# Optimization experiments

Measured on AMD Instinct MI355X. Metric: run time of the kernel, lower is better.

The kernel has to match this reference:

```python
import jax, jax.numpy as jnp
import numpy as np

D_MODEL = 1024
N_HEADS = 16
D_K = 64
BATCH = 2
SEQ = 2048
LN_EPS = 1e-5


def setup_inputs() -> dict:
    key = jax.random.key(0)
    ks = jax.random.split(key, 6)
    s = 1.0 / np.sqrt(D_MODEL)
    return {
        "h": jax.random.normal(ks[0], (BATCH, SEQ, D_MODEL), dtype=jnp.float32),
        "Wq": jax.random.normal(ks[1], (D_MODEL, D_MODEL), dtype=jnp.float32) * s,
        "bq": jnp.zeros((D_MODEL,), jnp.float32),
        "Wk": jax.random.normal(ks[2], (D_MODEL, D_MODEL), dtype=jnp.float32) * s,
        "bk": jnp.zeros((D_MODEL,), jnp.float32),
        "Wv": jax.random.normal(ks[3], (D_MODEL, D_MODEL), dtype=jnp.float32) * s,
        "bv": jnp.zeros((D_MODEL,), jnp.float32),
        "Wo": jax.random.normal(ks[4], (D_MODEL, D_MODEL), dtype=jnp.float32) * s,
        "bo": jnp.zeros((D_MODEL,), jnp.float32),
        "ln_w": jnp.ones((D_MODEL,), jnp.float32),
        "ln_b": jnp.zeros((D_MODEL,), jnp.float32),
    }


def _layernorm(x, w, b):
    mu = jnp.mean(x, axis=-1, keepdims=True)
    var = jnp.var(x, axis=-1, keepdims=True)
    return (x - mu) * jax.lax.rsqrt(var + LN_EPS) * w + b


def reference(h, Wq, bq, Wk, bk, Wv, bv, Wo, bo, ln_w, ln_b):
    b, s, _ = h.shape
    scale = 1.0 / np.sqrt(D_K)
    h_res = h
    hn = _layernorm(h, ln_w, ln_b)
    # Linear layers (torch convention: y = x @ W.T + b), split into heads
    q = (hn @ Wq.T + bq).reshape(b, s, N_HEADS, D_K)
    k = (hn @ Wk.T + bk).reshape(b, s, N_HEADS, D_K)
    v = (hn @ Wv.T + bv).reshape(b, s, N_HEADS, D_K)
    attn = jnp.einsum('bihd,bjhd->bhij', q, k) * scale  # [b, h, i, j]
    attn = jax.nn.softmax(attn, axis=-1)
    o = jnp.einsum('bhij,bjhd->bihd', attn, v).reshape(b, s, N_HEADS * D_K)
    out = o @ Wo.T + bo
    return out + h_res
```

## Files before the change

kernel.cpp:

```cpp
#include <hip/hip_runtime.h>
#include <cstdint>

#define D_MODEL 1024
#define N_HEADS 16
#define D_K     64
#define BATCH   2
#define SEQ     2048
#define TOKENS  (BATCH * SEQ)
#define LN_EPS  1e-5f
#define QSCALE  0.18033688011112042f

typedef __bf16 bf16x8 __attribute__((ext_vector_type(8)));
typedef float  floatx4  __attribute__((ext_vector_type(4)));
typedef float  floatx16 __attribute__((ext_vector_type(16)));

__device__ __forceinline__ unsigned short f2bf(float f) {
  union { float f; unsigned u; } v; v.f = f;
  unsigned r = v.u + 0x7fffu + ((v.u >> 16) & 1u);
  return (unsigned short)(r >> 16);
}
__device__ __forceinline__ unsigned pk2bf(float hi, float lo) {
  union { float f; unsigned u; } a, b;
  a.f = hi; b.f = lo;
  return __builtin_amdgcn_perm(a.u, b.u, 0x07060302u);
}

__device__ __forceinline__ void cp16(void* lds, const void* g) {
  __builtin_amdgcn_global_load_lds(
      (__attribute__((address_space(1))) void*)g,
      (__attribute__((address_space(3))) void*)lds, 16, 0, 0);
}

__global__ __launch_bounds__(256) void prep_kernel(
    const float* __restrict__ h, const float* __restrict__ w0,
    const float* __restrict__ w1, const float* __restrict__ w2,
    const float* __restrict__ w3, const float* __restrict__ lw,
    const float* __restrict__ lb, unsigned short* __restrict__ Wcat,
    unsigned short* __restrict__ hn) {
  if (blockIdx.x < 4096) {
    int wsel = blockIdx.x >> 10;
    const float* s = (wsel == 0) ? w0 : (wsel == 1) ? w1 : (wsel == 2) ? w2 : w3;
    unsigned short* d = Wcat + ((size_t)wsel << 20);
    int i = ((blockIdx.x & 1023) << 8) + threadIdx.x;
    float4 v = reinterpret_cast<const float4*>(s)[i];
    ushort4 o;
    o.x = f2bf(v.x); o.y = f2bf(v.y); o.z = f2bf(v.z); o.w = f2bf(v.w);
    reinterpret_cast<ushort4*>(d)[i] = o;
    return;
  }
  int row = blockIdx.x - 4096;
  const float* x = h + (size_t)row * D_MODEL;
  float4 v = reinterpret_cast<const float4*>(x)[threadIdx.x];
  float s  = v.x + v.y + v.z + v.w;
  float s2 = v.x * v.x + v.y * v.y + v.z * v.z + v.w * v.w;
  for (int m = 1; m < 64; m <<= 1) {
    s  += __shfl_xor(s, m);
    s2 += __shfl_xor(s2, m);
  }
  __shared__ float ls[4], ls2[4];
  int wave = threadIdx.x >> 6;
  if ((threadIdx.x & 63) == 0) { ls[wave] = s; ls2[wave] = s2; }
  __syncthreads();
  s  = ls[0] + ls[1] + ls[2] + ls[3];
  s2 = ls2[0] + ls2[1] + ls2[2] + ls2[3];
  float mu  = s * (1.0f / D_MODEL);
  float var = s2 * (1.0f / D_MODEL) - mu * mu;
  float rs  = rsqrtf(var + LN_EPS);
  float4 wv = reinterpret_cast<const float4*>(lw)[threadIdx.x];
  float4 bv = reinterpret_cast<const float4*>(lb)[threadIdx.x];
  ushort4 o;
  o.x = f2bf((v.x - mu) * rs * wv.x + bv.x);
  o.y = f2bf((v.y - mu) * rs * wv.y + bv.y);
  o.z = f2bf((v.z - mu) * rs * wv.z + bv.z);
  o.w = f2bf((v.w - mu) * rs * wv.w + bv.w);
  reinterpret_cast<ushort4*>(hn + (size_t)row * D_MODEL)[threadIdx.x] = o;
}

__global__ __launch_bounds__(256) void gemm_qkv_kernel(
    const unsigned short* __restrict__ A, const unsigned short* __restrict__ Wcat,
    const float* __restrict__ bq, const float* __restrict__ bk,
    const float* __restrict__ bv,
    unsigned short* __restrict__ QK, unsigned short* __restrict__ VtG) {
  __shared__ unsigned short As[128 * 64];
  __shared__ unsigned short Bs[128 * 64];

  const int tid  = threadIdx.x;
  const int w    = tid >> 6;
  const int lane = tid & 63;
  const int l15  = lane & 15;
  const int quad = lane >> 4;
  const int sw   = l15 & 7;
  const int wm = (w >> 1) * 64;
  const int wn = (w & 1) * 64;
  const int bm = blockIdx.y * 128;
  const int bn = blockIdx.x * 128;

  const int srow = tid >> 3;
  const int swzc = (((tid & 7) ^ (srow & 7)) * 8);
  const unsigned short* ga = A    + (size_t)(bm + srow) * 1024 + swzc;
  const unsigned short* gb = Wcat + (size_t)(bn + srow) * 1024 + swzc;
  unsigned short* asl = As + w * 512;
  unsigned short* bsl = Bs + w * 512;

  floatx4 acc[4][4];
  for (int i = 0; i < 4; ++i)
    for (int j = 0; j < 4; ++j) acc[i][j] = {0.f, 0.f, 0.f, 0.f};

  for (int k0 = 0; k0 < 1024; k0 += 64) {
#pragma unroll
    for (int i = 0; i < 4; ++i) cp16(asl + i * 2048, ga + (size_t)i * 32 * 1024 + k0);
#pragma unroll
    for (int i = 0; i < 4; ++i) cp16(bsl + i * 2048, gb + (size_t)i * 32 * 1024 + k0);
    __syncthreads();
#pragma unroll
    for (int kb = 0; kb < 2; ++kb) {
      bf16x8 af[4], bfr[4];
#pragma unroll
      for (int mi = 0; mi < 4; ++mi)
        af[mi] = *reinterpret_cast<const bf16x8*>(
            As + (wm + mi * 16 + l15) * 64 + (((kb * 4 + quad) ^ sw) * 8));
#pragma unroll
      for (int ni = 0; ni < 4; ++ni)
        bfr[ni] = *reinterpret_cast<const bf16x8*>(
            Bs + (wn + ni * 16 + l15) * 64 + (((kb * 4 + quad) ^ sw) * 8));
#pragma unroll
      for (int mi = 0; mi < 4; ++mi)
#pragma unroll
        for (int ni = 0; ni < 4; ++ni)
          acc[mi][ni] = __builtin_amdgcn_mfma_f32_16x16x32_bf16(af[mi], bfr[ni], acc[mi][ni], 0, 0, 0);
    }
    __syncthreads();
  }

  const int wsel = blockIdx.x >> 3;
  if (wsel == 0) {
#pragma unroll
    for (int mi = 0; mi < 4; ++mi)
#pragma unroll
      for (int ni = 0; ni < 4; ++ni) {
        int col = bn + wn + ni * 16 + l15;
        float bb = bq[col];
#pragma unroll
        for (int r = 0; r < 4; ++r) {
          int row = bm + wm + mi * 16 + quad * 4 + r;
          QK[(size_t)row * 2048 + col] = f2bf((acc[mi][ni][r] + bb) * QSCALE);
        }
      }
  } else if (wsel == 1) {
#pragma unroll
    for (int mi = 0; mi < 4; ++mi)
#pragma unroll
      for (int ni = 0; ni < 4; ++ni) {
        int col = bn + wn + ni * 16 + l15;
        float bb = bk[col - 1024];
#pragma unroll
        for (int r = 0; r < 4; ++r) {
          int row = bm + wm + mi * 16 + quad * 4 + r;
          QK[(size_t)row * 2048 + col] = f2bf(acc[mi][ni][r] + bb);
        }
      }
  } else {
#pragma unroll
    for (int mi = 0; mi < 4; ++mi)
#pragma unroll
      for (int ni = 0; ni < 4; ++ni) {
        int d = bn + wn + ni * 16 + l15 - 2048;
        float bb = bv[d];
        ushort4 o;
        o.x = f2bf(acc[mi][ni][0] + bb);
        o.y = f2bf(acc[mi][ni][1] + bb);
        o.z = f2bf(acc[mi][ni][2] + bb);
        o.w = f2bf(acc[mi][ni][3] + bb);
        int row0 = bm + wm + mi * 16 + quad * 4;
        *reinterpret_cast<ushort4*>(VtG + (size_t)d * 4096 + row0) = o;
      }
  }
}

__global__ __launch_bounds__(256) void gemm_out_kernel(
    const unsigned short* __restrict__ A, const unsigned short* __restrict__ Bt,
    const float* __restrict__ bo, const float* __restrict__ resid,
    float* __restrict__ out) {
  __shared__ unsigned short As[128 * 64];
  __shared__ unsigned short Bs[64 * 64];

  const int tid  = threadIdx.x;
  const int w    = tid >> 6;
  const int lane = tid & 63;
  const int l15  = lane & 15;
  const int quad = lane >> 4;
  const int sw   = l15 & 7;
  const int wm = (w >> 1) * 64;
  const int wn = (w & 1) * 32;
  const int bm = blockIdx.y * 128;
  const int bn = blockIdx.x * 64;

  const int srow = tid >> 3;
  const int swzc = (((tid & 7) ^ (srow & 7)) * 8);
  const unsigned short* ga = A  + (size_t)(bm + srow) * 1024 + swzc;
  const unsigned short* gb = Bt + (size_t)(bn + srow) * 1024 + swzc;
  unsigned short* asl = As + w * 512;
  unsigned short* bsl = Bs + w * 512;

  floatx4 acc[4][2];
  for (int i = 0; i < 4; ++i)
    for (int j = 0; j < 2; ++j) acc[i][j] = {0.f, 0.f, 0.f, 0.f};

  for (int k0 = 0; k0 < 1024; k0 += 64) {
#pragma unroll
    for (int i = 0; i < 4; ++i) cp16(asl + i * 2048, ga + (size_t)i * 32 * 1024 + k0);
#pragma unroll
    for (int i = 0; i < 2; ++i) cp16(bsl + i * 2048, gb + (size_t)i * 32 * 1024 + k0);
    __syncthreads();
#pragma unroll
    for (int kb = 0; kb < 2; ++kb) {
      bf16x8 af[4], bfr[2];
#pragma unroll
      for (int mi = 0; mi < 4; ++mi)
        af[mi] = *reinterpret_cast<const bf16x8*>(
            As + (wm + mi * 16 + l15) * 64 + (((kb * 4 + quad) ^ sw) * 8));
#pragma unroll
      for (int ni = 0; ni < 2; ++ni)
        bfr[ni] = *reinterpret_cast<const bf16x8*>(
            Bs + (wn + ni * 16 + l15) * 64 + (((kb * 4 + quad) ^ sw) * 8));
#pragma unroll
      for (int mi = 0; mi < 4; ++mi)
#pragma unroll
        for (int ni = 0; ni < 2; ++ni)
          acc[mi][ni] = __builtin_amdgcn_mfma_f32_16x16x32_bf16(af[mi], bfr[ni], acc[mi][ni], 0, 0, 0);
    }
    __syncthreads();
  }

#pragma unroll
  for (int mi = 0; mi < 4; ++mi)
#pragma unroll
    for (int ni = 0; ni < 2; ++ni) {
      int col = bn + wn + ni * 16 + l15;
      float bb = bo[col];
#pragma unroll
      for (int r = 0; r < 4; ++r) {
        int row = bm + wm + mi * 16 + quad * 4 + r;
        size_t idx = (size_t)row * 1024 + col;
        out[idx] = acc[mi][ni][r] + bb + resid[idx];
      }
    }
}

__global__ __launch_bounds__(256) void attn_kernel(
    const unsigned short* __restrict__ QK, const unsigned short* __restrict__ VtG,
    unsigned short* __restrict__ O) {
  __shared__ unsigned short Ks[2][128 * 64];
  __shared__ unsigned short Vs[2][64 * 128];

  const int tid  = threadIdx.x;
  const int w    = tid >> 6;
  const int lane = tid & 63;
  const int l31  = lane & 31;
  const int h    = lane >> 5;
  const int s7   = l31 & 7;

  const int hh = blockIdx.x, qt = blockIdx.y, bz = blockIdx.z;
  const int tq0  = bz * SEQ + qt * 128;
  const int hoff = hh * 64;

  bf16x8 qf[4];
  {
    const unsigned short* qp =
        QK + (size_t)(tq0 + w * 32 + l31) * 2048 + hoff + h * 8;
#pragma unroll
    for (int kd = 0; kd < 4; ++kd)
      qf[kd] = *reinterpret_cast<const bf16x8*>(qp + kd * 16);
  }

  floatx16 oacc[2];
#pragma unroll
  for (int db = 0; db < 2; ++db)
#pragma unroll
    for (int r = 0; r < 16; ++r) oacc[db][r] = 0.f;
  float lsum = 0.f;

  const unsigned short* kg = QK + 1024 + hoff
      + (size_t)(bz * SEQ + (tid >> 3)) * 2048
      + (((tid & 7) ^ ((tid >> 3) & 7)) * 8);
  const unsigned short* vg = VtG
      + (size_t)(hoff + (tid >> 4)) * 4096 + bz * SEQ
      + (((tid & 15) ^ ((tid >> 4) & 7)) * 8);

  auto stage = [&](int kt, int b) {
    const unsigned short* kgi = kg + (size_t)(kt * 128) * 2048;
    const unsigned short* vgi = vg + kt * 128;
    unsigned short* ksl = Ks[b] + w * 512;
    unsigned short* vsl = Vs[b] + w * 512;
#pragma unroll
    for (int i = 0; i < 4; ++i) cp16(ksl + i * 2048, kgi + (size_t)(i * 32) * 2048);
#pragma unroll
    for (int i = 0; i < 4; ++i) cp16(vsl + i * 2048, vgi + (size_t)(i * 16) * 4096);
  };

  stage(0, 0);

  for (int kt = 0; kt < SEQ / 128; ++kt) {
    __syncthreads();
    if (kt + 1 < SEQ / 128) stage(kt + 1, (kt + 1) & 1);
    const unsigned short* Kb = Ks[kt & 1];
    const unsigned short* Vb = Vs[kt & 1];

    floatx16 ss[4];
#pragma unroll
    for (int kb = 0; kb < 4; ++kb)
#pragma unroll
      for (int r = 0; r < 16; ++r) ss[kb][r] = 0.f;
#pragma unroll
    for (int kb = 0; kb < 4; ++kb) {
      const unsigned short* krow = Kb + (kb * 32 + l31) * 64;
#pragma unroll
      for (int kd = 0; kd < 4; ++kd) {
        bf16x8 kf = *reinterpret_cast<const bf16x8*>(
            krow + (((kd * 2 + h) ^ s7) * 8));
        ss[kb] = __builtin_amdgcn_mfma_f32_32x32x16_bf16(kf, qf[kd], ss[kb], 0, 0, 0);
      }
    }

#pragma unroll
    for (int kb = 0; kb < 4; ++kb) {
      float e[16];
      float bs = 0.f;
#pragma unroll
      for (int r = 0; r < 16; ++r) {
        e[r] = __builtin_amdgcn_exp2f(ss[kb][r]);
        bs += e[r];
      }
      bs += __shfl_xor(bs, 32);
      lsum += bs;
      unsigned p[8];
#pragma unroll
      for (int i = 0; i < 8; ++i) p[i] = pk2bf(e[2 * i + 1], e[2 * i]);

#pragma unroll
      for (int sub = 0; sub < 2; ++sub) {
        unsigned pl0 = p[sub * 4 + 0], pl1 = p[sub * 4 + 1];
        unsigned ph0 = p[sub * 4 + 2], ph1 = p[sub * 4 + 3];
        unsigned rec0 = __shfl_xor((int)(h ? pl0 : ph0), 32);
        unsigned rec1 = __shfl_xor((int)(h ? pl1 : ph1), 32);
        union { unsigned u[4]; bf16x8 v; } pf;
        pf.u[0] = h ? rec0 : pl0;
        pf.u[1] = h ? rec1 : pl1;
        pf.u[2] = h ? ph0 : rec0;
        pf.u[3] = h ? ph1 : rec1;
#pragma unroll
        for (int db = 0; db < 2; ++db) {
          bf16x8 vf = *reinterpret_cast<const bf16x8*>(
              Vb + (db * 32 + l31) * 128 + (((kb * 4 + sub * 2 + h) ^ s7) * 8));
          oacc[db] = __builtin_amdgcn_mfma_f32_32x32x16_bf16(vf, pf.v, oacc[db], 0, 0, 0);
        }
      }
    }
  }

  float inv = 1.0f / lsum;
  unsigned short* ob = O + (size_t)(tq0 + w * 32 + l31) * 1024 + hoff;
#pragma unroll
  for (int db = 0; db < 2; ++db)
#pragma unroll
    for (int rg = 0; rg < 4; ++rg) {
      int d0 = db * 32 + rg * 8 + h * 4;
      uint2 ov;
      ov.x = pk2bf(oacc[db][rg * 4 + 1] * inv, oacc[db][rg * 4 + 0] * inv);
      ov.y = pk2bf(oacc[db][rg * 4 + 3] * inv, oacc[db][rg * 4 + 2] * inv);
      *reinterpret_cast<uint2*>(ob + d0) = ov;
    }
}

extern "C" void kernel_launch(void* const* d_in, const int* in_sizes, int n_in,
                              void* d_out, int out_size, void* d_ws, size_t ws_size,
                              hipStream_t stream) {
  const float* h    = (const float*)d_in[0];
  const float* Wq   = (const float*)d_in[1];
  const float* bq   = (const float*)d_in[2];
  const float* Wk   = (const float*)d_in[3];
  const float* bk   = (const float*)d_in[4];
  const float* Wv   = (const float*)d_in[5];
  const float* bv   = (const float*)d_in[6];
  const float* Wo   = (const float*)d_in[7];
  const float* bo   = (const float*)d_in[8];
  const float* ln_w = (const float*)d_in[9];
  const float* ln_b = (const float*)d_in[10];
  float* out = (float*)d_out;

  unsigned short* ws = (unsigned short*)d_ws;
  const size_t WSZ = (size_t)1 << 20;
  unsigned short* Wcat = ws;
  unsigned short* hn   = Wcat + 4 * WSZ;
  unsigned short* QKb  = hn + (size_t)TOKENS * D_MODEL;
  unsigned short* VtG  = QKb + (size_t)TOKENS * 2048;
  unsigned short* Obuf = VtG + (size_t)D_MODEL * TOKENS;

  prep_kernel<<<8192, 256, 0, stream>>>(h, Wq, Wk, Wv, Wo, ln_w, ln_b, Wcat, hn);

  gemm_qkv_kernel<<<dim3(24, 32), 256, 0, stream>>>(hn, Wcat, bq, bk, bv, QKb, VtG);

  attn_kernel<<<dim3(N_HEADS, SEQ / 128, BATCH), 256, 0, stream>>>(QKb, VtG, Obuf);

  gemm_out_kernel<<<dim3(16, 32), 256, 0, stream>>>(Obuf, Wcat + 3 * WSZ, bo, h, out);
}
```

Before: 200.8 us.

## Split attention key blocks across two wave groups and reduce partials in LDS

Doubles the attention block to 512 threads. Each of four query-row wave slots gets a second wave, and the two split the four 32-key sub-blocks of every tile, so each wave computes half the QK and PV MFMAs. At the end, the upper waves write their partial O accumulators and row sums into LDS, reusing the K/V buffers, and the lower waves add them in and normalize. The goal is more waves per CU to hide latency and shorter per-wave dependency chains, at the cost of an extra LDS reduction and barriers.

```diff
diff --git a/kernel.cpp b/kernel.cpp
--- a/kernel.cpp
+++ b/kernel.cpp
@@ -247,7 +247,7 @@
     }
 }
 
-__global__ __launch_bounds__(256) void attn_kernel(
+__global__ __launch_bounds__(512, 4) void attn_kernel(
     const unsigned short* __restrict__ QK, const unsigned short* __restrict__ VtG,
     unsigned short* __restrict__ O) {
   __shared__ unsigned short Ks[2][128 * 64];
@@ -255,6 +255,8 @@
 
   const int tid  = threadIdx.x;
   const int w    = tid >> 6;
+  const int wq   = w & 3;
+  const int kb0  = (w >> 2) * 2;
   const int lane = tid & 63;
   const int l31  = lane & 31;
   const int h    = lane >> 5;
@@ -267,7 +269,7 @@
   bf16x8 qf[4];
   {
     const unsigned short* qp =
-        QK + (size_t)(tq0 + w * 32 + l31) * 2048 + hoff + h * 8;
+        QK + (size_t)(tq0 + wq * 32 + l31) * 2048 + hoff + h * 8;
 #pragma unroll
     for (int kd = 0; kd < 4; ++kd)
       qf[kd] = *reinterpret_cast<const bf16x8*>(qp + kd * 16);
@@ -293,9 +295,9 @@
     unsigned short* ksl = Ks[b] + w * 512;
     unsigned short* vsl = Vs[b] + w * 512;
 #pragma unroll
-    for (int i = 0; i < 4; ++i) cp16(ksl + i * 2048, kgi + (size_t)(i * 32) * 2048);
-#pragma unroll
-    for (int i = 0; i < 4; ++i) cp16(vsl + i * 2048, vgi + (size_t)(i * 16) * 4096);
+    for (int i = 0; i < 2; ++i) cp16(ksl + i * 4096, kgi + (size_t)(i * 64) * 2048);
+#pragma unroll
+    for (int i = 0; i < 2; ++i) cp16(vsl + i * 4096, vgi + (size_t)(i * 32) * 4096);
   };
 
   stage(0, 0);
@@ -306,29 +308,31 @@
     const unsigned short* Kb = Ks[kt & 1];
     const unsigned short* Vb = Vs[kt & 1];
 
-    floatx16 ss[4];
-#pragma unroll
-    for (int kb = 0; kb < 4; ++kb)
-#pragma unroll
-      for (int r = 0; r < 16; ++r) ss[kb][r] = 0.f;
-#pragma unroll
-    for (int kb = 0; kb < 4; ++kb) {
+    floatx16 ss[2];
+#pragma unroll
+    for (int kk = 0; kk < 2; ++kk)
+#pragma unroll
+      for (int r = 0; r < 16; ++r) ss[kk][r] = 0.f;
+#pragma unroll
+    for (int kk = 0; kk < 2; ++kk) {
+      const int kb = kb0 + kk;
       const unsigned short* krow = Kb + (kb * 32 + l31) * 64;
 #pragma unroll
       for (int kd = 0; kd < 4; ++kd) {
         bf16x8 kf = *reinterpret_cast<const bf16x8*>(
             krow + (((kd * 2 + h) ^ s7) * 8));
-        ss[kb] = __builtin_amdgcn_mfma_f32_32x32x16_bf16(kf, qf[kd], ss[kb], 0, 0, 0);
+        ss[kk] = __builtin_amdgcn_mfma_f32_32x32x16_bf16(kf, qf[kd], ss[kk], 0, 0, 0);
       }
     }
 
 #pragma unroll
-    for (int kb = 0; kb < 4; ++kb) {
+    for (int kk = 0; kk < 2; ++kk) {
+      const int kb = kb0 + kk;
       float e[16];
       float bs = 0.f;
 #pragma unroll
       for (int r = 0; r < 16; ++r) {
-        e[r] = __builtin_amdgcn_exp2f(ss[kb][r]);
+        e[r] = __builtin_amdgcn_exp2f(ss[kk][r]);
         bs += e[r];
       }
       bs += __shfl_xor(bs, 32);
@@ -358,18 +362,41 @@
     }
   }
 
-  float inv = 1.0f / lsum;
-  unsigned short* ob = O + (size_t)(tq0 + w * 32 + l31) * 1024 + hoff;
-#pragma unroll
-  for (int db = 0; db < 2; ++db)
-#pragma unroll
-    for (int rg = 0; rg < 4; ++rg) {
-      int d0 = db * 32 + rg * 8 + h * 4;
-      uint2 ov;
-      ov.x = pk2bf(oacc[db][rg * 4 + 1] * inv, oacc[db][rg * 4 + 0] * inv);
-      ov.y = pk2bf(oacc[db][rg * 4 + 3] * inv, oacc[db][rg * 4 + 2] * inv);
-      *reinterpret_cast<uint2*>(ob + d0) = ov;
-    }
+  __syncthreads();
+  float* osc = (float*)&Ks[0][0];
+  float* lsc = (float*)&Vs[0][0];
+  if (w >= 4) {
+    float* dst = osc + ((size_t)(wq * 64 + lane) * 32);
+#pragma unroll
+    for (int db = 0; db < 2; ++db)
+#pragma unroll
+      for (int r = 0; r < 16; ++r)
+        dst[(db * 16 + r + lane) & 31] = oacc[db][r];
+    lsc[wq * 64 + lane] = lsum;
+  }
+  __syncthreads();
+  if (w < 4) {
+    const float* src = osc + ((size_t)(wq * 64 + lane) * 32);
+    lsum += lsc[wq * 64 + lane];
+#pragma unroll
+    for (int db = 0; db < 2; ++db)
+#pragma unroll
+      for (int r = 0; r < 16; ++r)
+        oacc[db][r] += src[(db * 16 + r + lane) & 31];
+
+    float inv = 1.0f / lsum;
+    unsigned short* ob = O + (size_t)(tq0 + wq * 32 + l31) * 1024 + hoff;
+#pragma unroll
+    for (int db = 0; db < 2; ++db)
+#pragma unroll
+      for (int rg = 0; rg < 4; ++rg) {
+        int d0 = db * 32 + rg * 8 + h * 4;
+        uint2 ov;
+        ov.x = pk2bf(oacc[db][rg * 4 + 1] * inv, oacc[db][rg * 4 + 0] * inv);
+        ov.y = pk2bf(oacc[db][rg * 4 + 3] * inv, oacc[db][rg * 4 + 2] * inv);
+        *reinterpret_cast<uint2*>(ob + d0) = ov;
+      }
+  }
 }
 
 extern "C" void kernel_launch(void* const* d_in, const int* in_sizes, int n_in,
@@ -400,7 +427,7 @@
 
   gemm_qkv_kernel<<<dim3(24, 32), 256, 0, stream>>>(hn, Wcat, bq, bk, bv, QKb, VtG);
 
-  attn_kernel<<<dim3(N_HEADS, SEQ / 128, BATCH), 256, 0, stream>>>(QKb, VtG, Obuf);
+  attn_kernel<<<dim3(N_HEADS, SEQ / 128, BATCH), 512, 0, stream>>>(QKb, VtG, Obuf);
 
   gemm_out_kernel<<<dim3(16, 32), 256, 0, stream>>>(Obuf, Wcat + 3 * WSZ, bo, h, out);
 }
```

After: 198.1 us. About the same (-1.3%).
